# Performance work log

Hardware: AMD Instinct MI355X
Metric: run time of the kernel (lower is better)

The kernel has to match this reference:

```python
import jax, jax.numpy as jnp
import numpy as np


def setup_inputs() -> dict:
    key = jax.random.key(0)
    kq, kk, kv = jax.random.split(key, 3)
    L, D = 8192, 64
    return {
        "q": jax.random.normal(kq, (L, D), dtype=jnp.float32),
        "k": jax.random.normal(kk, (L, D), dtype=jnp.float32),
        "v": jax.random.normal(kv, (L, D), dtype=jnp.float32),
    }


def reference(q, k, v):
    # score = q @ k^T  (NOTE: source applies no 1/sqrt(d) scaling)
    score = jnp.einsum("qd,kd->qk", q, k)          # [Lq, Lk]
    score = jax.nn.softmax(score, axis=-1)          # row-wise softmax
    out = jnp.einsum("qk,kd->qd", score, v)         # [Lq, D]
    return (out, score)
```

## Files before the change

### kernel.cpp

```cpp
#include <hip/hip_runtime.h>

#define LSEQ 8192
#define DDIM 64
#define SHIFT 20.0f
#define QTILE 128
#define KC 64

#define KSPL1 16
#define KRANGE1 (LSEQ / KSPL1)
#define KSPL2 8
#define KRANGE2 (LSEQ / KSPL2)

#define VSTR 72
#define PSTR 68

typedef __attribute__((ext_vector_type(8))) short bf16x8;
typedef __attribute__((ext_vector_type(4))) float f32x4;

#define MFMA16(a, b, c) __builtin_amdgcn_mfma_f32_16x16x32_bf16(a, b, c, 0, 0, 0)

__device__ inline short f2bf(float x) {
    unsigned u = __float_as_uint(x);
    u += 0x7FFF + ((u >> 16) & 1);
    return (short)(u >> 16);
}

__device__ inline void split8(float4 a, float4 b, bf16x8& hi, bf16x8& lo) {
    float t[8] = {a.x, a.y, a.z, a.w, b.x, b.y, b.z, b.w};
#pragma unroll
    for (int j = 0; j < 8; ++j) {
        unsigned u  = __float_as_uint(t[j]);
        unsigned hu = u & 0xFFFF0000u;
        hi[j] = (short)(hu >> 16);
        lo[j] = f2bf(t[j] - __uint_as_float(hu));
    }
}

#define QK_TILE(acc, khB, klB, R)                                                   \
    {                                                                               \
        const int   sw  = ((R) & 7) << 4;                                           \
        const char* khb = (khB) + (R) * 128;                                        \
        const char* klb = (klB) + (R) * 128;                                        \
        bf16x8 kh0 = *(const bf16x8*)(khb + ((quad * 16) ^ sw));                    \
        bf16x8 kh1 = *(const bf16x8*)(khb + ((64 + quad * 16) ^ sw));               \
        bf16x8 kl0 = *(const bf16x8*)(klb + ((quad * 16) ^ sw));                    \
        bf16x8 kl1 = *(const bf16x8*)(klb + ((64 + quad * 16) ^ sw));               \
        acc = MFMA16(qh[s][0], kh0, acc);                                           \
        acc = MFMA16(qh[s][1], kh1, acc);                                           \
        acc = MFMA16(ql[s][0], kh0, acc);                                           \
        acc = MFMA16(ql[s][1], kh1, acc);                                           \
        acc = MFMA16(qh[s][0], kl0, acc);                                           \
        acc = MFMA16(qh[s][1], kl1, acc);                                           \
    }

#define K_ISSUE(kc_)                                                                \
    { _Pragma("unroll") for (int ii = 0; ii < 2; ++ii) {                            \
        int s_ = ii * 256 + tid; int kk = s_ >> 3, dseg = s_ & 7;                   \
        const float* kp = kptr + (size_t)(kb + (kc_) + kk) * DDIM + dseg * 8;       \
        pk0[ii] = *(const float4*)kp; pk1[ii] = *(const float4*)(kp + 4); } }

#define K_COMMIT(khB, klB)                                                          \
    { _Pragma("unroll") for (int ii = 0; ii < 2; ++ii) {                            \
        int s_ = ii * 256 + tid; int kk = s_ >> 3, dseg = s_ & 7;                   \
        bf16x8 hi, lo; split8(pk0[ii], pk1[ii], hi, lo);                            \
        int off = kk * 128 + ((dseg * 16) ^ ((kk & 7) << 4));                       \
        *(bf16x8*)((khB) + off) = hi; *(bf16x8*)((klB) + off) = lo; } }

#define V_ISSUE(kc_)                                                                \
    { _Pragma("unroll") for (int ii = 0; ii < 4; ++ii) {                            \
        int e4 = (ii * 256 + tid) * 4; int d = e4 & 63, kl2 = e4 >> 6;              \
        pvv[ii] = *(const float4*)(vptr + (size_t)(kb + (kc_) + kl2) * DDIM + d); } }

#define V_COMMIT(vtB)                                                               \
    { _Pragma("unroll") for (int ii = 0; ii < 4; ++ii) {                            \
        int e4 = (ii * 256 + tid) * 4; int d = e4 & 63, kl2 = e4 >> 6;              \
        (vtB)[(d + 0) * VSTR + kl2] = (unsigned short)f2bf(pvv[ii].x);              \
        (vtB)[(d + 1) * VSTR + kl2] = (unsigned short)f2bf(pvv[ii].y);              \
        (vtB)[(d + 2) * VSTR + kl2] = (unsigned short)f2bf(pvv[ii].z);              \
        (vtB)[(d + 3) * VSTR + kl2] = (unsigned short)f2bf(pvv[ii].w); } }

#define Q_FRAGS()                                                                   \
    { _Pragma("unroll") for (int s = 0; s < 2; ++s) {                               \
        const float* qp = q + (size_t)(q0 + wave * 32 + s * 16 + r) * DDIM;         \
        float4 a = *(const float4*)(qp + quad * 8);                                 \
        float4 b = *(const float4*)(qp + quad * 8 + 4);                             \
        split8(a, b, qh[s][0], ql[s][0]);                                           \
        a = *(const float4*)(qp + 32 + quad * 8);                                   \
        b = *(const float4*)(qp + 32 + quad * 8 + 4);                               \
        split8(a, b, qh[s][1], ql[s][1]); } }

__global__ __launch_bounds__(256, 4) void sdpa_rowsum(
    const float* __restrict__ q, const float* __restrict__ k, float* __restrict__ l)
{
    const int tid = threadIdx.x, lane = tid & 63, wave = tid >> 6;
    const int quad = lane >> 4, r = lane & 15;
    const int q0 = blockIdx.x * QTILE, kb = blockIdx.y * KRANGE1;
    const float* kptr = k;

    __shared__ __align__(16) char KhiS[2][KC * 128];
    __shared__ __align__(16) char KloS[2][KC * 128];

    bf16x8 qh[2][2], ql[2][2];
    Q_FRAGS();

    float4 pk0[2], pk1[2];
    K_ISSUE(0);
    K_COMMIT(KhiS[0], KloS[0]);
    K_ISSUE(KC);
    __syncthreads();

    float esum[2][4];
#pragma unroll
    for (int s = 0; s < 2; ++s)
#pragma unroll
        for (int i = 0; i < 4; ++i) esum[s][i] = 0.f;

    const int NCH = KRANGE1 / KC;
    for (int c = 0; c < NCH; ++c) {
        const char* khB = KhiS[c & 1];
        const char* klB = KloS[c & 1];
        __builtin_amdgcn_s_setprio(1);
#pragma unroll
        for (int s = 0; s < 2; ++s) {
#pragma unroll
            for (int kt = 0; kt < KC / 16; ++kt) {
                const int R = kt * 16 + r;
                f32x4 acc = {0.f, 0.f, 0.f, 0.f};
                QK_TILE(acc, khB, klB, R);
#pragma unroll
                for (int i = 0; i < 4; ++i) esum[s][i] += __expf(acc[i] - SHIFT);
            }
        }
        __builtin_amdgcn_s_setprio(0);
        if (c + 1 < NCH) K_COMMIT(KhiS[(c + 1) & 1], KloS[(c + 1) & 1]);
        if (c + 2 < NCH) K_ISSUE((c + 2) * KC);
        __syncthreads();
    }

#pragma unroll
    for (int s = 0; s < 2; ++s)
#pragma unroll
        for (int i = 0; i < 4; ++i) {
#pragma unroll
            for (int off = 1; off < 16; off <<= 1)
                esum[s][i] += __shfl_xor(esum[s][i], off);
        }
    if (r == 0) {
#pragma unroll
        for (int s = 0; s < 2; ++s)
#pragma unroll
            for (int i = 0; i < 4; ++i)
                atomicAdd(&l[q0 + wave * 32 + s * 16 + quad * 4 + i], esum[s][i]);
    }
}

__global__ __launch_bounds__(256, 2) void sdpa_score_pv(
    const float* __restrict__ q, const float* __restrict__ k, const float* __restrict__ v,
    const float* __restrict__ l, float* __restrict__ outp, float* __restrict__ score)
{
    const int tid = threadIdx.x, lane = tid & 63, wave = tid >> 6;
    const int quad = lane >> 4, r = lane & 15;
    const int q0 = blockIdx.x * QTILE, kb = blockIdx.y * KRANGE2;
    const float* kptr = k;
    const float* vptr = v;

    __shared__ __align__(16) char KhiS[2][KC * 128];
    __shared__ __align__(16) char KloS[2][KC * 128];
    __shared__ __align__(16) unsigned short VTS[2][DDIM * VSTR];
    __shared__ __align__(16) unsigned short PLS[4][32 * PSTR];

    bf16x8 qh[2][2], ql[2][2];
    Q_FRAGS();

    float  lr[2][4];
    size_t rowbase[2][4];
#pragma unroll
    for (int s = 0; s < 2; ++s)
#pragma unroll
        for (int i = 0; i < 4; ++i) {
            int qrow      = q0 + wave * 32 + s * 16 + quad * 4 + i;
            lr[s][i]      = 1.0f / l[qrow];
            rowbase[s][i] = (size_t)qrow * LSEQ + kb;
        }

    unsigned short* Pl = PLS[wave];
    f32x4 accpv[2][4];
#pragma unroll
    for (int s = 0; s < 2; ++s)
#pragma unroll
        for (int nb = 0; nb < 4; ++nb) accpv[s][nb] = (f32x4){0.f, 0.f, 0.f, 0.f};

    float4 pk0[2], pk1[2], pvv[4];
    K_ISSUE(0);
    V_ISSUE(0);
    K_COMMIT(KhiS[0], KloS[0]);
    V_COMMIT(VTS[0]);
    K_ISSUE(KC);
    V_ISSUE(KC);
    __syncthreads();

    const int NCH = KRANGE2 / KC;
    for (int c = 0; c < NCH; ++c) {
        const int kc = c * KC;
        const char* khB = KhiS[c & 1];
        const char* klB = KloS[c & 1];
        const unsigned short* vtB = VTS[c & 1];

        __builtin_amdgcn_s_setprio(1);
#pragma unroll
        for (int s = 0; s < 2; ++s) {
#pragma unroll
            for (int kt = 0; kt < KC / 16; ++kt) {
                const int R = kt * 16 + r;
                f32x4 acc = {0.f, 0.f, 0.f, 0.f};
                QK_TILE(acc, khB, klB, R);
#pragma unroll
                for (int i = 0; i < 4; ++i) {
                    float p = __expf(acc[i] - SHIFT) * lr[s][i];
                    __builtin_nontemporal_store(p, &score[rowbase[s][i] + kc + kt * 16 + r]);
                    Pl[(s * 16 + quad * 4 + i) * PSTR + kt * 16 + r] = (unsigned short)f2bf(p);
                }
            }
        }
#pragma unroll
        for (int s = 0; s < 2; ++s) {
#pragma unroll
            for (int ks = 0; ks < 2; ++ks) {
                bf16x8 af = *(const bf16x8*)(&Pl[(s * 16 + r) * PSTR + ks * 32 + quad * 8]);
#pragma unroll
                for (int nb = 0; nb < 4; ++nb) {
                    bf16x8 bf_ = *(const bf16x8*)(&vtB[(nb * 16 + r) * VSTR + ks * 32 + quad * 8]);
                    accpv[s][nb] = MFMA16(af, bf_, accpv[s][nb]);
                }
            }
        }
        __builtin_amdgcn_s_setprio(0);

        if (c + 1 < NCH) {
            K_COMMIT(KhiS[(c + 1) & 1], KloS[(c + 1) & 1]);
            V_COMMIT(VTS[(c + 1) & 1]);
        }
        if (c + 2 < NCH) { K_ISSUE((c + 2) * KC); V_ISSUE((c + 2) * KC); }
        __syncthreads();
    }

#pragma unroll
    for (int s = 0; s < 2; ++s)
#pragma unroll
        for (int nb = 0; nb < 4; ++nb)
#pragma unroll
            for (int i = 0; i < 4; ++i) {
                int qrow = q0 + wave * 32 + s * 16 + quad * 4 + i;
                atomicAdd(&outp[(size_t)qrow * DDIM + nb * 16 + r], accpv[s][nb][i]);
            }
}

extern "C" void kernel_launch(void* const* d_in, const int* in_sizes, int n_in,
                              void* d_out, int out_size, void* d_ws, size_t ws_size,
                              hipStream_t stream) {
    const float* q = (const float*)d_in[0];
    const float* k = (const float*)d_in[1];
    const float* v = (const float*)d_in[2];
    float* out   = (float*)d_out;
    float* score = out + (size_t)LSEQ * DDIM;
    float* l     = (float*)d_ws;

    hipMemsetAsync(l, 0, LSEQ * sizeof(float), stream);
    hipMemsetAsync(out, 0, (size_t)LSEQ * DDIM * sizeof(float), stream);

    sdpa_rowsum  <<<dim3(LSEQ / QTILE, KSPL1), 256, 0, stream>>>(q, k, l);
    sdpa_score_pv<<<dim3(LSEQ / QTILE, KSPL2), 256, 0, stream>>>(q, k, v, l, out, score);
}
```

Baseline: 403.8 us.

## Swap MFMA operands for row-contiguous scores, reuse K/V fragments, swizzle V tile

The QK MFMA now takes K as the A operand and Q as the B operand. Each lane then holds four consecutive key columns of one query row, so score writes become 16-byte vector nontemporal stores and P writes into LDS become 8-byte stores. The loops are reordered so each K fragment load serves both query subtiles and each V fragment serves both subtiles in PV. The V transpose tile gets an XOR swizzle to reduce LDS bank conflicts, and the rowsum reduction shrinks to two shuffles with one atomic per row per lane group. The risk is more register pressure from keeping fragments live, and a correctness dependence on the swizzled V addressing matching between writes and reads.

```diff
diff --git a/kernel.cpp b/kernel.cpp
--- a/kernel.cpp
+++ b/kernel.cpp
@@ -16,6 +16,7 @@
 
 typedef __attribute__((ext_vector_type(8))) short bf16x8;
 typedef __attribute__((ext_vector_type(4))) float f32x4;
+typedef __attribute__((ext_vector_type(4))) unsigned short u16x4;
 
 #define MFMA16(a, b, c) __builtin_amdgcn_mfma_f32_16x16x32_bf16(a, b, c, 0, 0, 0)
 
@@ -36,22 +37,27 @@
     }
 }
 
-#define QK_TILE(acc, khB, klB, R)                                                   \
-    {                                                                               \
-        const int   sw  = ((R) & 7) << 4;                                           \
-        const char* khb = (khB) + (R) * 128;                                        \
-        const char* klb = (klB) + (R) * 128;                                        \
-        bf16x8 kh0 = *(const bf16x8*)(khb + ((quad * 16) ^ sw));                    \
-        bf16x8 kh1 = *(const bf16x8*)(khb + ((64 + quad * 16) ^ sw));               \
-        bf16x8 kl0 = *(const bf16x8*)(klb + ((quad * 16) ^ sw));                    \
-        bf16x8 kl1 = *(const bf16x8*)(klb + ((64 + quad * 16) ^ sw));               \
-        acc = MFMA16(qh[s][0], kh0, acc);                                           \
-        acc = MFMA16(qh[s][1], kh1, acc);                                           \
-        acc = MFMA16(ql[s][0], kh0, acc);                                           \
-        acc = MFMA16(ql[s][1], kh1, acc);                                           \
-        acc = MFMA16(qh[s][0], kl0, acc);                                           \
-        acc = MFMA16(qh[s][1], kl1, acc);                                           \
-    }
+__device__ inline int vt_addr(int d, int k) {
+    return d * (VSTR * 2) + ((k * 2) ^ ((d & 7) << 4));
+}
+
+#define K_FRAGS(kt)                                                                 \
+    const int   R   = (kt) * 16 + r;                                                \
+    const int   sw  = (R & 7) << 4;                                                 \
+    const char* khb = khB + R * 128;                                                \
+    const char* klb = klB + R * 128;                                                \
+    bf16x8 kh0 = *(const bf16x8*)(khb + ((quad * 16) ^ sw));                        \
+    bf16x8 kh1 = *(const bf16x8*)(khb + ((64 + quad * 16) ^ sw));                   \
+    bf16x8 kl0 = *(const bf16x8*)(klb + ((quad * 16) ^ sw));                        \
+    bf16x8 kl1 = *(const bf16x8*)(klb + ((64 + quad * 16) ^ sw));
+
+#define QK_SWAP(acc, s)                                                             \
+    acc = MFMA16(kh0, qh[s][0], acc);                                               \
+    acc = MFMA16(kh1, qh[s][1], acc);                                               \
+    acc = MFMA16(kh0, ql[s][0], acc);                                               \
+    acc = MFMA16(kh1, ql[s][1], acc);                                               \
+    acc = MFMA16(kl0, qh[s][0], acc);                                               \
+    acc = MFMA16(kl1, qh[s][1], acc);
 
 #define K_ISSUE(kc_)                                                                \
     { _Pragma("unroll") for (int ii = 0; ii < 2; ++ii) {                            \
@@ -59,25 +65,25 @@
         const float* kp = kptr + (size_t)(kb + (kc_) + kk) * DDIM + dseg * 8;       \
         pk0[ii] = *(const float4*)kp; pk1[ii] = *(const float4*)(kp + 4); } }
 
-#define K_COMMIT(khB, klB)                                                          \
+#define K_COMMIT(khB_, klB_)                                                        \
     { _Pragma("unroll") for (int ii = 0; ii < 2; ++ii) {                            \
         int s_ = ii * 256 + tid; int kk = s_ >> 3, dseg = s_ & 7;                   \
         bf16x8 hi, lo; split8(pk0[ii], pk1[ii], hi, lo);                            \
         int off = kk * 128 + ((dseg * 16) ^ ((kk & 7) << 4));                       \
-        *(bf16x8*)((khB) + off) = hi; *(bf16x8*)((klB) + off) = lo; } }
+        *(bf16x8*)((khB_) + off) = hi; *(bf16x8*)((klB_) + off) = lo; } }
 
 #define V_ISSUE(kc_)                                                                \
     { _Pragma("unroll") for (int ii = 0; ii < 4; ++ii) {                            \
         int e4 = (ii * 256 + tid) * 4; int d = e4 & 63, kl2 = e4 >> 6;              \
         pvv[ii] = *(const float4*)(vptr + (size_t)(kb + (kc_) + kl2) * DDIM + d); } }
 
-#define V_COMMIT(vtB)                                                               \
+#define V_COMMIT(vtB_)                                                              \
     { _Pragma("unroll") for (int ii = 0; ii < 4; ++ii) {                            \
         int e4 = (ii * 256 + tid) * 4; int d = e4 & 63, kl2 = e4 >> 6;              \
-        (vtB)[(d + 0) * VSTR + kl2] = (unsigned short)f2bf(pvv[ii].x);              \
-        (vtB)[(d + 1) * VSTR + kl2] = (unsigned short)f2bf(pvv[ii].y);              \
-        (vtB)[(d + 2) * VSTR + kl2] = (unsigned short)f2bf(pvv[ii].z);              \
-        (vtB)[(d + 3) * VSTR + kl2] = (unsigned short)f2bf(pvv[ii].w); } }
+        *(unsigned short*)((vtB_) + vt_addr(d + 0, kl2)) = (unsigned short)f2bf(pvv[ii].x); \
+        *(unsigned short*)((vtB_) + vt_addr(d + 1, kl2)) = (unsigned short)f2bf(pvv[ii].y); \
+        *(unsigned short*)((vtB_) + vt_addr(d + 2, kl2)) = (unsigned short)f2bf(pvv[ii].z); \
+        *(unsigned short*)((vtB_) + vt_addr(d + 3, kl2)) = (unsigned short)f2bf(pvv[ii].w); } }
 
 #define Q_FRAGS()                                                                   \
     { _Pragma("unroll") for (int s = 0; s < 2; ++s) {                               \
@@ -109,11 +115,7 @@
     K_ISSUE(KC);
     __syncthreads();
 
-    float esum[2][4];
-#pragma unroll
-    for (int s = 0; s < 2; ++s)
-#pragma unroll
-        for (int i = 0; i < 4; ++i) esum[s][i] = 0.f;
+    float esum[2] = {0.f, 0.f};
 
     const int NCH = KRANGE1 / KC;
     for (int c = 0; c < NCH; ++c) {
@@ -121,14 +123,14 @@
         const char* klB = KloS[c & 1];
         __builtin_amdgcn_s_setprio(1);
 #pragma unroll
-        for (int s = 0; s < 2; ++s) {
-#pragma unroll
-            for (int kt = 0; kt < KC / 16; ++kt) {
-                const int R = kt * 16 + r;
+        for (int kt = 0; kt < KC / 16; ++kt) {
+            K_FRAGS(kt)
+#pragma unroll
+            for (int s = 0; s < 2; ++s) {
                 f32x4 acc = {0.f, 0.f, 0.f, 0.f};
-                QK_TILE(acc, khB, klB, R);
-#pragma unroll
-                for (int i = 0; i < 4; ++i) esum[s][i] += __expf(acc[i] - SHIFT);
+                QK_SWAP(acc, s)
+#pragma unroll
+                for (int i = 0; i < 4; ++i) esum[s] += __expf(acc[i] - SHIFT);
             }
         }
         __builtin_amdgcn_s_setprio(0);
@@ -138,19 +140,11 @@
     }
 
 #pragma unroll
-    for (int s = 0; s < 2; ++s)
-#pragma unroll
-        for (int i = 0; i < 4; ++i) {
-#pragma unroll
-            for (int off = 1; off < 16; off <<= 1)
-                esum[s][i] += __shfl_xor(esum[s][i], off);
-        }
-    if (r == 0) {
-#pragma unroll
-        for (int s = 0; s < 2; ++s)
-#pragma unroll
-            for (int i = 0; i < 4; ++i)
-                atomicAdd(&l[q0 + wave * 32 + s * 16 + quad * 4 + i], esum[s][i]);
+    for (int s = 0; s < 2; ++s) {
+        float v = esum[s];
+        v += __shfl_xor(v, 16);
+        v += __shfl_xor(v, 32);
+        if (lane < 16) atomicAdd(&l[q0 + wave * 32 + s * 16 + lane], v);
     }
 }
 
@@ -166,22 +160,20 @@
 
     __shared__ __align__(16) char KhiS[2][KC * 128];
     __shared__ __align__(16) char KloS[2][KC * 128];
-    __shared__ __align__(16) unsigned short VTS[2][DDIM * VSTR];
+    __shared__ __align__(16) char VTS[2][DDIM * VSTR * 2];
     __shared__ __align__(16) unsigned short PLS[4][32 * PSTR];
 
     bf16x8 qh[2][2], ql[2][2];
     Q_FRAGS();
 
-    float  lr[2][4];
-    size_t rowbase[2][4];
-#pragma unroll
-    for (int s = 0; s < 2; ++s)
-#pragma unroll
-        for (int i = 0; i < 4; ++i) {
-            int qrow      = q0 + wave * 32 + s * 16 + quad * 4 + i;
-            lr[s][i]      = 1.0f / l[qrow];
-            rowbase[s][i] = (size_t)qrow * LSEQ + kb;
-        }
+    float  lr[2];
+    size_t rowbase[2];
+#pragma unroll
+    for (int s = 0; s < 2; ++s) {
+        int qrow   = q0 + wave * 32 + s * 16 + r;
+        lr[s]      = 1.0f / l[qrow];
+        rowbase[s] = (size_t)qrow * LSEQ + kb;
+    }
 
     unsigned short* Pl = PLS[wave];
     f32x4 accpv[2][4];
@@ -204,34 +196,43 @@
         const int kc = c * KC;
         const char* khB = KhiS[c & 1];
         const char* klB = KloS[c & 1];
-        const unsigned short* vtB = VTS[c & 1];
+        const char* vtB = VTS[c & 1];
 
         __builtin_amdgcn_s_setprio(1);
 #pragma unroll
-        for (int s = 0; s < 2; ++s) {
-#pragma unroll
-            for (int kt = 0; kt < KC / 16; ++kt) {
-                const int R = kt * 16 + r;
+        for (int kt = 0; kt < KC / 16; ++kt) {
+            K_FRAGS(kt)
+#pragma unroll
+            for (int s = 0; s < 2; ++s) {
                 f32x4 acc = {0.f, 0.f, 0.f, 0.f};
-                QK_TILE(acc, khB, klB, R);
-#pragma unroll
-                for (int i = 0; i < 4; ++i) {
-                    float p = __expf(acc[i] - SHIFT) * lr[s][i];
-                    __builtin_nontemporal_store(p, &score[rowbase[s][i] + kc + kt * 16 + r]);
-                    Pl[(s * 16 + quad * 4 + i) * PSTR + kt * 16 + r] = (unsigned short)f2bf(p);
-                }
-            }
-        }
-#pragma unroll
-        for (int s = 0; s < 2; ++s) {
-#pragma unroll
-            for (int ks = 0; ks < 2; ++ks) {
+                QK_SWAP(acc, s)
+                f32x4 pq;
+                u16x4 pb;
+                pq.x = __expf(acc[0] - SHIFT) * lr[s];
+                pq.y = __expf(acc[1] - SHIFT) * lr[s];
+                pq.z = __expf(acc[2] - SHIFT) * lr[s];
+                pq.w = __expf(acc[3] - SHIFT) * lr[s];
+                pb.x = (unsigned short)f2bf(pq.x);
+                pb.y = (unsigned short)f2bf(pq.y);
+                pb.z = (unsigned short)f2bf(pq.z);
+                pb.w = (unsigned short)f2bf(pq.w);
+                __builtin_nontemporal_store(pq,
+                    (f32x4*)(score + rowbase[s] + kc + kt * 16 + quad * 4));
+                *(u16x4*)(&Pl[(s * 16 + r) * PSTR + kt * 16 + quad * 4]) = pb;
+            }
+        }
+#pragma unroll
+        for (int ks = 0; ks < 2; ++ks) {
+            bf16x8 vb[4];
+#pragma unroll
+            for (int nb = 0; nb < 4; ++nb)
+                vb[nb] = *(const bf16x8*)(vtB + vt_addr(nb * 16 + r, ks * 32 + quad * 8));
+#pragma unroll
+            for (int s = 0; s < 2; ++s) {
                 bf16x8 af = *(const bf16x8*)(&Pl[(s * 16 + r) * PSTR + ks * 32 + quad * 8]);
 #pragma unroll
-                for (int nb = 0; nb < 4; ++nb) {
-                    bf16x8 bf_ = *(const bf16x8*)(&vtB[(nb * 16 + r) * VSTR + ks * 32 + quad * 8]);
-                    accpv[s][nb] = MFMA16(af, bf_, accpv[s][nb]);
-                }
+                for (int nb = 0; nb < 4; ++nb)
+                    accpv[s][nb] = MFMA16(af, vb[nb], accpv[s][nb]);
             }
         }
         __builtin_amdgcn_s_setprio(0);
```

New measurement: 425.3 us. 1.05x slower.
